# Optimization experiments

Hardware: AMD Instinct MI355X
Metric: run time of the kernel (lower is better)

The kernel has to match this reference:

```python
import jax, jax.numpy as jnp
import numpy as np
from jax import lax
from jax.scipy.special import logsumexp

B, S, H = 64, 512, 768
NUM_TAG, NUM_POS = 17, 45


def setup_inputs() -> dict:
    key = jax.random.key(0)
    ks = jax.random.split(key, 12)
    return {
        "hidden": jax.random.normal(ks[0], (B, S, H), dtype=jnp.float32),
        "mask": jnp.ones((B, S), dtype=jnp.int32),
        "target_tag": jax.random.randint(ks[1], (B, S), 0, NUM_TAG).astype(jnp.int64),
        "target_pos": jax.random.randint(ks[2], (B, S), 0, NUM_POS).astype(jnp.int64),
        "W_tag": jax.random.normal(ks[3], (H, NUM_TAG), dtype=jnp.float32) * 0.02,
        "b_tag": jnp.zeros((NUM_TAG,), dtype=jnp.float32),
        "W_pos": jax.random.normal(ks[4], (H, NUM_POS), dtype=jnp.float32) * 0.02,
        "b_pos": jnp.zeros((NUM_POS,), dtype=jnp.float32),
        "start_tag": jax.random.normal(ks[5], (NUM_TAG,), dtype=jnp.float32) * 0.1,
        "trans_tag": jax.random.normal(ks[6], (NUM_TAG, NUM_TAG), dtype=jnp.float32) * 0.1,
        "end_tag": jax.random.normal(ks[7], (NUM_TAG,), dtype=jnp.float32) * 0.1,
        "start_pos": jax.random.normal(ks[8], (NUM_POS,), dtype=jnp.float32) * 0.1,
        "trans_pos": jax.random.normal(ks[9], (NUM_POS, NUM_POS), dtype=jnp.float32) * 0.1,
        "end_pos": jax.random.normal(ks[10], (NUM_POS,), dtype=jnp.float32) * 0.1,
    }


def crf_nll(emissions, tags, mask, start, trans, end):
    """torchcrf negative log-likelihood, reduction='mean'. emissions:[B,S,T]."""
    e = jnp.swapaxes(emissions, 0, 1)            # [S,B,T]
    tg = jnp.swapaxes(tags, 0, 1)                # [S,B]
    m = jnp.swapaxes(mask, 0, 1).astype(emissions.dtype)  # [S,B]
    # --- numerator: score of the target path ---
    first = start[tg[0]] + jnp.take_along_axis(e[0], tg[0][:, None], 1)[:, 0]

    def num_step(carry, x):
        prev_tag, score = carry
        et, tt, mt = x
        s = trans[prev_tag, tt] + jnp.take_along_axis(et, tt[:, None], 1)[:, 0]
        score = score + s * mt
        prev_tag = jnp.where(mt > 0, tt, prev_tag)
        return (prev_tag, score), None

    (last_tag, num), _ = lax.scan(num_step, (tg[0], first), (e[1:], tg[1:], m[1:]))
    num = num + end[last_tag]
    # --- denominator: forward algorithm (log-sum-exp scan) ---
    score0 = start[None, :] + e[0]               # [B,T]

    def den_step(score, x):
        et, mt = x
        nxt = logsumexp(score[:, :, None] + trans[None, :, :] + et[:, None, :], axis=1)
        return jnp.where(mt[:, None] > 0, nxt, score), None

    den, _ = lax.scan(den_step, score0, (e[1:], m[1:]))
    den = logsumexp(den + end[None, :], axis=1)
    return -jnp.mean(num - den)


def crf_decode(emissions, mask, start, trans, end):
    """Viterbi decode; returns best tag paths [B,S] (int32)."""
    T = emissions.shape[-1]
    e = jnp.swapaxes(emissions, 0, 1)            # [S,B,T]
    m = jnp.swapaxes(mask, 0, 1)                 # [S,B]
    score0 = start[None, :] + e[0]

    def fwd_step(score, x):
        et, mt = x
        cand = score[:, :, None] + trans[None, :, :]     # [B,T,T]
        idx = jnp.argmax(cand, axis=1).astype(jnp.int32)  # [B,T] best prev tag
        nxt = jnp.max(cand, axis=1) + et
        keep = (mt > 0)[:, None]
        score = jnp.where(keep, nxt, score)
        idx = jnp.where(keep, idx, jnp.arange(T, dtype=jnp.int32)[None, :])
        return score, idx

    score, hist = lax.scan(fwd_step, score0, (e[1:], m[1:]))  # hist:[S-1,B,T]
    score = score + end[None, :]
    last = jnp.argmax(score, axis=1).astype(jnp.int32)        # [B]

    def back_step(tag, idx):
        prev = jnp.take_along_axis(idx, tag[:, None], 1)[:, 0]
        return prev, tag

    tag0, path = lax.scan(back_step, last, hist, reverse=True)  # path:[S-1,B]
    full = jnp.concatenate([tag0[None, :], path], axis=0)       # [S,B]
    return jnp.swapaxes(full, 0, 1)


def reference(hidden, mask, target_tag, target_pos,
              W_tag, b_tag, W_pos, b_pos,
              start_tag, trans_tag, end_tag,
              start_pos, trans_pos, end_pos):
    # dropout is identity in eval mode
    tag = jnp.einsum('bsh,ht->bst', hidden, W_tag) + b_tag   # [B,S,T]
    pos = jnp.einsum('bsh,hp->bsp', hidden, W_pos) + b_pos   # [B,S,P]
    loss_tag = crf_nll(jax.nn.log_softmax(tag, axis=2), target_tag, mask,
                       start_tag, trans_tag, end_tag)
    loss_pos = crf_nll(jax.nn.log_softmax(pos, axis=2), target_pos, mask,
                       start_pos, trans_pos, end_pos)
    pred_tag = crf_decode(tag, mask, start_tag, trans_tag, end_tag)
    pred_pos = crf_decode(pos, mask, start_pos, trans_pos, end_pos)
    return pred_tag, pred_pos, loss_tag, loss_pos
```

## Files before the change

### kernel.cpp

```cpp
#include <hip/hip_runtime.h>
#include <cmath>
#include <cstdint>
#include <cstddef>

#define NT 17
#define NP 45
#define CH 8

__device__ __forceinline__ float rlane(float v, int k) {
    return __int_as_float(__builtin_amdgcn_readlane(__float_as_int(v), k));
}

__device__ __forceinline__ float bperm(float v, int k) {
    return __int_as_float(__builtin_amdgcn_ds_bpermute(k * 4, __float_as_int(v)));
}

__device__ __forceinline__ void gload16(const float* g, float* l) {
    __builtin_amdgcn_global_load_lds(
        (const __attribute__((address_space(1))) void*)g,
        (__attribute__((address_space(3))) void*)l, 16, 0, 0);
}

__global__ __launch_bounds__(256) void pack_w(
    const float* __restrict__ Wt, const float* __restrict__ Wp,
    float* __restrict__ Wpk)
{
    int i = blockIdx.x * 256 + threadIdx.x;
    if (i >= 768 * 64) return;
    int k = i >> 6, c = i & 63;
    float v = 0.f;
    if (c < NT) v = Wt[k * NT + c];
    else if (c < NT + NP) v = Wp[k * NP + (c - NT)];
    Wpk[i] = v;
}

__global__ __launch_bounds__(256) void gemm_logits(
    const float* __restrict__ hidden, const float* __restrict__ Wpk,
    const float* __restrict__ bt, const float* __restrict__ bp,
    float* __restrict__ tagL, float* __restrict__ posL)
{
    __shared__ __align__(16) float As[64 * 32];
    __shared__ __align__(16) float Bs[32 * 64];
    const int tid = threadIdx.x;
    const int rg = tid >> 4;
    const int cg = tid & 15;
    const int srg = rg & 7;
    const int row0 = blockIdx.x * 64;

    float acc[4][4];
#pragma unroll
    for (int a = 0; a < 4; ++a)
#pragma unroll
        for (int b = 0; b < 4; ++b) acc[a][b] = 0.f;

    const int arow = tid >> 3;
    const int aq   = tid & 7;
    const int bk   = tid >> 4;
    const int bc4  = tid & 15;

#pragma unroll 1
    for (int kc = 0; kc < 768; kc += 32) {
        {
            int r0 = arow;
            int s0 = (r0 >> 2) & 7;
            gload16(hidden + (size_t)(row0 + r0) * 768 + kc + ((aq ^ s0) << 2),
                    As + r0 * 32 + aq * 4);
            int r1 = 32 + arow;
            int s1 = (r1 >> 2) & 7;
            gload16(hidden + (size_t)(row0 + r1) * 768 + kc + ((aq ^ s1) << 2),
                    As + r1 * 32 + aq * 4);
            gload16(Wpk + (size_t)(kc + bk) * 64 + bc4 * 4,
                    Bs + bk * 64 + bc4 * 4);
            gload16(Wpk + (size_t)(kc + 16 + bk) * 64 + bc4 * 4,
                    Bs + (16 + bk) * 64 + bc4 * 4);
        }
        __syncthreads();
#pragma unroll
        for (int k4 = 0; k4 < 8; ++k4) {
            const int qb = ((k4 ^ srg) << 2);
            float a_[4][4], b_[4][4];
#pragma unroll
            for (int jr = 0; jr < 4; ++jr) {
                float4 t = *(const float4*)(As + (rg * 4 + jr) * 32 + qb);
                a_[jr][0] = t.x; a_[jr][1] = t.y; a_[jr][2] = t.z; a_[jr][3] = t.w;
            }
#pragma unroll
            for (int kk = 0; kk < 4; ++kk) {
                float4 t = *(const float4*)(Bs + (k4 * 4 + kk) * 64 + cg * 4);
                b_[kk][0] = t.x; b_[kk][1] = t.y; b_[kk][2] = t.z; b_[kk][3] = t.w;
            }
#pragma unroll
            for (int kk = 0; kk < 4; ++kk)
#pragma unroll
                for (int jr = 0; jr < 4; ++jr)
#pragma unroll
                    for (int jc = 0; jc < 4; ++jc)
                        acc[jr][jc] = fmaf(a_[jr][kk], b_[kk][jc], acc[jr][jc]);
        }
        __syncthreads();
    }
#pragma unroll
    for (int jr = 0; jr < 4; ++jr) {
        size_t r = (size_t)row0 + rg * 4 + jr;
#pragma unroll
        for (int jc = 0; jc < 4; ++jc) {
            int c = cg * 4 + jc;
            if (c < NT) tagL[r * NT + c] = acc[jr][jc] + bt[c];
            else if (c < NT + NP) posL[r * NP + (c - NT)] = acc[jr][jc] + bp[c - NT];
        }
    }
}

template <int T, int PAD>
__device__ void nll_scan(int b,
    const float* __restrict__ logits, const int* __restrict__ mask,
    const int* __restrict__ targ, const float* __restrict__ start,
    const float* __restrict__ trans, const float* __restrict__ endv,
    float* __restrict__ den, float* __restrict__ num)
{
    const int lane = threadIdx.x;
    const int jj = (lane < T) ? lane : (T - 1);
    float Ecol[PAD];
#pragma unroll
    for (int i = 0; i < PAD; ++i) Ecol[i] = (i < T) ? __expf(trans[i * T + jj]) : 0.f;
    const float esjj = __expf(start[jj]);
    const float* eptr = logits + (size_t)b * 512 * T + jj;
    const int* mptr = mask + b * 512;

    float eb[CH], en[CH], fb[CH];
    int mb, mn = 0;
#pragma unroll
    for (int k = 0; k < CH; ++k) { eb[k] = eptr[k * T]; en[k] = 0.f; }
    mb = mptr[lane & (CH - 1)];

    float a = 0.f;
    int excorr = 0;
    for (int c = 0; c < 64; ++c) {
        unsigned long long kb = __ballot(mb > 0);
        if (c < 63) {
            const float* ep2 = eptr + (c + 1) * CH * T;
#pragma unroll
            for (int k = 0; k < CH; ++k) en[k] = ep2[k * T];
            mn = mptr[(c + 1) * CH + (lane & (CH - 1))];
        }
#pragma unroll
        for (int k = 0; k < CH; ++k) fb[k] = __expf(eb[k]);
#pragma unroll
        for (int s = 0; s < CH; ++s) {
            float bv[PAD];
#pragma unroll
            for (int i = 0; i < PAD; ++i) bv[i] = bperm(a, i);
            float d0 = 0.f, d1 = 0.f, d2 = 0.f, d3 = 0.f;
#pragma unroll
            for (int q = 0; q < PAD / 4; ++q) {
                d0 = fmaf(bv[4 * q + 0], Ecol[4 * q + 0], d0);
                d1 = fmaf(bv[4 * q + 1], Ecol[4 * q + 1], d1);
                d2 = fmaf(bv[4 * q + 2], Ecol[4 * q + 2], d2);
                d3 = fmaf(bv[4 * q + 3], Ecol[4 * q + 3], d3);
            }
            float cand = ((d0 + d1) + (d2 + d3)) * fb[s];
            bool keep = (kb >> s) & 1ULL;
            bool first = (c == 0) && (s == 0);
            a = first ? (esjj * fb[0]) : (keep ? cand : a);
        }
        float mv0 = rlane(a, 0), mv1 = rlane(a, 1);
        float mv2 = rlane(a, 2), mv3 = rlane(a, 3);
#pragma unroll
        for (int i = 4; i < T; i += 4) {
            mv0 = fmaxf(mv0, rlane(a, i + 0));
            mv1 = fmaxf(mv1, rlane(a, i + 1));
            mv2 = fmaxf(mv2, rlane(a, i + 2));
            mv3 = fmaxf(mv3, rlane(a, i + 3));
        }
        float m = fmaxf(fmaxf(mv0, mv1), fmaxf(mv2, mv3));
        int ex;
        (void)frexpf(m, &ex);
        a *= ldexpf(1.0f, -ex);
        excorr += ex;
#pragma unroll
        for (int k = 0; k < CH; ++k) eb[k] = en[k];
        mb = mn;
    }
    float term = (lane < T) ? a * __expf(endv[lane]) : 0.f;
#pragma unroll
    for (int o = 32; o; o >>= 1) term += __shfl_xor(term, o);
    if (lane == 0) den[b] = __logf(term) + (float)excorr * 0.69314718056f;

    float part = 0.f; int Lc = 0;
    for (int t = lane; t < 512; t += 64) {
        int mt = mask[b * 512 + t];
        Lc += (mt > 0);
        if (t >= 1 && mt > 0) {
            int tg = targ[b * 512 + t];
            int pg = targ[b * 512 + t - 1];
            part += trans[pg * T + tg] + logits[((size_t)b * 512 + t) * T + tg];
        }
    }
#pragma unroll
    for (int o = 32; o; o >>= 1) { part += __shfl_xor(part, o); Lc += __shfl_xor(Lc, o); }
    if (lane == 0) {
        int t0g = targ[b * 512];
        num[b] = start[t0g] + logits[(size_t)b * 512 * T + t0g]
               + part + endv[targ[b * 512 + Lc - 1]];
    }
}

template <int T, int PAD>
__device__ void vit_fwd(int b,
    const float* __restrict__ logits, const int* __restrict__ mask,
    const float* __restrict__ start, const float* __restrict__ trans,
    float* __restrict__ score)
{
    const int lane = threadIdx.x;
    const int jj = (lane < T) ? lane : (T - 1);
    float Tcol[PAD];
#pragma unroll
    for (int i = 0; i < PAD; ++i) Tcol[i] = (i < T) ? trans[i * T + jj] : -1e30f;
    const float sjj = start[jj];
    const float* eptr = logits + (size_t)b * 512 * T + jj;
    const int* mptr = mask + b * 512;
    float* sptr = score + (size_t)b * 512 * T + lane;

    float eb[CH], en[CH];
    int mb, mn = 0;
#pragma unroll
    for (int k = 0; k < CH; ++k) { eb[k] = eptr[k * T]; en[k] = 0.f; }
    mb = mptr[lane & (CH - 1)];

    float sc = 0.f;
    for (int c = 0; c < 64; ++c) {
        unsigned long long kb = __ballot(mb > 0);
        if (c < 63) {
            const float* ep2 = eptr + (c + 1) * CH * T;
#pragma unroll
            for (int k = 0; k < CH; ++k) en[k] = ep2[k * T];
            mn = mptr[(c + 1) * CH + (lane & (CH - 1))];
        }
#pragma unroll
        for (int s = 0; s < CH; ++s) {
            float bv[PAD];
#pragma unroll
            for (int i = 0; i < PAD; ++i) bv[i] = bperm(sc, i);
            float m = -1e30f;
#pragma unroll
            for (int q = 0; q < PAD / 4; ++q) {
                float ca = bv[4 * q + 0] + Tcol[4 * q + 0];
                float cb = bv[4 * q + 1] + Tcol[4 * q + 1];
                float cc = bv[4 * q + 2] + Tcol[4 * q + 2];
                float cd = bv[4 * q + 3] + Tcol[4 * q + 3];
                m = fmaxf(m, fmaxf(ca, cb));
                m = fmaxf(m, fmaxf(cc, cd));
            }
            float nxt = m + eb[s];
            bool keep = (kb >> s) & 1ULL;
            bool first = (c == 0) && (s == 0);
            sc = first ? (sjj + eb[0]) : (keep ? nxt : sc);
            if (lane < T) sptr[(size_t)(c * CH + s) * T] = sc;
        }
#pragma unroll
        for (int k = 0; k < CH; ++k) eb[k] = en[k];
        mb = mn;
    }
}

__global__ __launch_bounds__(64, 1) void scan_kernel(
    const float* tagL, const float* posL, const int* mask,
    const int* tgT, const int* tgP,
    const float* startT, const float* transT, const float* endT,
    const float* startP, const float* transP, const float* endP,
    float* scoreT, float* scoreP,
    float* denT, float* denP, float* numT, float* numP)
{
    int bid = blockIdx.x;
    if (bid < 64)
        vit_fwd<NP, 48>(bid, posL, mask, startP, transP, scoreP);
    else if (bid < 128)
        nll_scan<NP, 48>(bid - 64, posL, mask, tgP, startP, transP, endP, denP, numP);
    else if (bid < 192)
        vit_fwd<NT, 20>(bid - 128, tagL, mask, startT, transT, scoreT);
    else
        nll_scan<NT, 20>(bid - 192, tagL, mask, tgT, startT, transT, endT, denT, numT);
}

template <int T>
__device__ void hist_block(int b, int tc,
    const float* __restrict__ score, const int* __restrict__ mask,
    const float* __restrict__ trans, unsigned char* __restrict__ hist)
{
    const int wave = threadIdx.x >> 6;
    const int lane = threadIdx.x & 63;
    const int jj = (lane < T) ? lane : (T - 1);
    float Tcol[T];
#pragma unroll
    for (int i = 0; i < T; ++i) Tcol[i] = trans[i * T + jj];
    for (int q = 0; q < 16; ++q) {
        int t = tc * 64 + wave * 16 + q;
        if (t < 1) continue;
        int mt = mask[b * 512 + t];
        int hv;
        if (mt > 0) {
            float sv = score[((size_t)b * 512 + t - 1) * T + jj];
            float mx = -1e30f; int am = 0;
#pragma unroll
            for (int i = 0; i < T; ++i) {
                float cand = rlane(sv, i) + Tcol[i];
                bool g = cand > mx;
                mx = g ? cand : mx;
                am = g ? i : am;
            }
            hv = am;
        } else {
            hv = jj;
        }
        if (lane < T)
            hist[((size_t)b * 512 + (t - 1)) * T + lane] = (unsigned char)hv;
    }
}

__global__ __launch_bounds__(256) void hist_kernel(
    const float* scoreT, const float* scoreP, const int* mask,
    const float* transT, const float* transP,
    unsigned char* histT, unsigned char* histP)
{
    int blk = blockIdx.x;
    if (blk < 512) hist_block<NP>(blk >> 3, blk & 7, scoreP, mask, transP, histP);
    else { blk -= 512; hist_block<NT>(blk >> 3, blk & 7, scoreT, mask, transT, histT); }
}

template <int T>
__device__ void backtrace(int b, const float* __restrict__ score,
    const unsigned char* __restrict__ hist, const float* __restrict__ endv,
    float* __restrict__ outp, unsigned char* sh)
{
    unsigned char* h  = sh;
    unsigned char* g2 = sh + 512 * T;
    unsigned char* g4 = sh + 1024 * T;
    unsigned char* g8 = sh + 1024 * T + 128 * T;
    unsigned char* pr = sh + 1024 * T + 192 * T;
    const int lane = threadIdx.x;

    {
        const int4* src = (const int4*)(hist + (size_t)b * 512 * T);
        int4* dst = (int4*)h;
        int n16 = (512 * T) / 16;
        for (int i = lane; i < n16; i += 64) dst[i] = src[i];
    }
    __syncthreads();
    for (int idx = lane; idx < 510 * T; idx += 64) {
        int r = idx / T, i = idx - r * T;
        g2[idx] = h[r * T + h[(r + 1) * T + i]];
    }
    __syncthreads();
    for (int idx = lane; idx < 127 * T; idx += 64) {
        int a4 = idx / T, i = idx - a4 * T;
        int r = 3 + 4 * a4;
        g4[idx] = g2[r * T + g2[(r + 2) * T + i]];
    }
    __syncthreads();
    for (int idx = lane; idx < 63 * T; idx += 64) {
        int a = idx / T, i = idx - a * T;
        int r = 503 - 8 * a;
        int a4lo = (r - 3) >> 2, a4hi = (r + 1) >> 2;
        g8[idx] = g4[a4lo * T + g4[a4hi * T + i]];
    }
    float v = (lane < T) ? (score[((size_t)b * 512 + 511) * T + lane] + endv[lane]) : -1e30f;
    float mx = v;
#pragma unroll
    for (int o = 32; o; o >>= 1) mx = fmaxf(mx, __shfl_xor(mx, o));
    unsigned long long bal = __ballot(v == mx);
    int cur = __ffsll(bal) - 1;
    __syncthreads();
    int myCur = 0;
    for (int a = 0; a < 64; ++a) {
        if (lane == a) myCur = cur;
        if (a < 63) cur = g8[a * T + cur];
    }
    {
        int ta = 511 - 8 * lane;
        int j = myCur;
        pr[ta] = (unsigned char)j;
        int rlo = (lane == 63) ? 0 : (ta - 7);
        for (int r = ta - 1; r >= rlo; --r) {
            j = h[r * T + j];
            pr[r] = (unsigned char)j;
        }
    }
    __syncthreads();
    for (int k = lane; k < 512; k += 64)
        outp[(size_t)b * 512 + k] = (float)pr[k];
}

__global__ __launch_bounds__(64, 1) void backtrace_kernel(
    const float* scoreT, const float* scoreP,
    const unsigned char* histT, const unsigned char* histP,
    const float* endT, const float* endP,
    const float* numT, const float* denT,
    const float* numP, const float* denP, float* out)
{
    __shared__ __align__(16) unsigned char sh[1216 * NP + 576];
    int blk = blockIdx.x;
    if (blk < 64) backtrace<NP>(blk, scoreP, histP, endP, out + 32768, sh);
    else if (blk < 128) backtrace<NT>(blk - 64, scoreT, histT, endT, out, sh);
    else {
        int lane = threadIdx.x;
        float dT = numT[lane] - denT[lane];
        float dP = numP[lane] - denP[lane];
#pragma unroll
        for (int o = 32; o; o >>= 1) { dT += __shfl_xor(dT, o); dP += __shfl_xor(dP, o); }
        if (lane == 0) {
            out[65536] = -dT / 64.f;
            out[65537] = -dP / 64.f;
        }
    }
}

extern "C" void kernel_launch(void* const* d_in, const int* in_sizes, int n_in,
                              void* d_out, int out_size, void* d_ws, size_t ws_size,
                              hipStream_t stream)
{
    const float* hidden = (const float*)d_in[0];
    const int*   mask   = (const int*)d_in[1];
    const int*   tgT    = (const int*)d_in[2];
    const int*   tgP    = (const int*)d_in[3];
    const float* Wt     = (const float*)d_in[4];
    const float* bt     = (const float*)d_in[5];
    const float* Wp     = (const float*)d_in[6];
    const float* bp     = (const float*)d_in[7];
    const float* startT = (const float*)d_in[8];
    const float* transT = (const float*)d_in[9];
    const float* endT   = (const float*)d_in[10];
    const float* startP = (const float*)d_in[11];
    const float* transP = (const float*)d_in[12];
    const float* endP   = (const float*)d_in[13];

    float* ws     = (float*)d_ws;
    float* tagL   = ws;
    float* posL   = tagL + 557056;
    float* scoreT = posL + 1474560;
    float* scoreP = scoreT + 557056;
    float* denT   = scoreP + 1474560;
    float* denP   = denT + 64;
    float* numT   = denP + 64;
    float* numP   = numT + 64;
    unsigned char* histT = (unsigned char*)(numP + 64);
    unsigned char* histP = histT + (size_t)64 * 512 * NT;
    float* out = (float*)d_out;

    float* Wpk = scoreT;

    pack_w<<<192, 256, 0, stream>>>(Wt, Wp, Wpk);
    gemm_logits<<<512, 256, 0, stream>>>(hidden, Wpk, bt, bp, tagL, posL);
    scan_kernel<<<256, 64, 0, stream>>>(tagL, posL, mask, tgT, tgP,
        startT, transT, endT, startP, transP, endP,
        scoreT, scoreP, denT, denP, numT, numP);
    hist_kernel<<<1024, 256, 0, stream>>>(scoreT, scoreP, mask, transT, transP,
        histT, histP);
    backtrace_kernel<<<129, 64, 0, stream>>>(scoreT, scoreP, histT, histP,
        endT, endP, numT, denT, numP, denP, out);
}
```

Baseline: 409.9 us.

## Fuse Viterbi backpointer argmax into forward scan and drop hist kernel

Result: slower. 494.1 us (+20.6%).

```diff
diff --git a/kernel.cpp b/kernel.cpp
--- a/kernel.cpp
+++ b/kernel.cpp
@@ -6,6 +6,7 @@
 #define NT 17
 #define NP 45
 #define CH 8
+#define HS 528
 
 __device__ __forceinline__ float rlane(float v, int k) {
     return __int_as_float(__builtin_amdgcn_readlane(__float_as_int(v), k));
@@ -209,8 +210,9 @@
 __device__ void vit_fwd(int b,
     const float* __restrict__ logits, const int* __restrict__ mask,
     const float* __restrict__ start, const float* __restrict__ trans,
-    float* __restrict__ score)
-{
+    float* __restrict__ scoreFin, unsigned char* __restrict__ histX)
+{
+    constexpr int L = PAD / 4;
     const int lane = threadIdx.x;
     const int jj = (lane < T) ? lane : (T - 1);
     float Tcol[PAD];
@@ -219,7 +221,7 @@
     const float sjj = start[jj];
     const float* eptr = logits + (size_t)b * 512 * T + jj;
     const int* mptr = mask + b * 512;
-    float* sptr = score + (size_t)b * 512 * T + lane;
+    unsigned char* hbase = histX + ((size_t)b * T + lane) * HS;
 
     float eb[CH], en[CH];
     int mb, mn = 0;
@@ -228,6 +230,7 @@
     mb = mptr[lane & (CH - 1)];
 
     float sc = 0.f;
+    unsigned int plo = 0, phi = 0;
     for (int c = 0; c < 64; ++c) {
         unsigned long long kb = __ballot(mb > 0);
         if (c < 63) {
@@ -241,25 +244,62 @@
             float bv[PAD];
 #pragma unroll
             for (int i = 0; i < PAD; ++i) bv[i] = bperm(sc, i);
+            float cnd[PAD];
+#pragma unroll
+            for (int i = 0; i < PAD; ++i) cnd[i] = bv[i] + Tcol[i];
             float m = -1e30f;
 #pragma unroll
             for (int q = 0; q < PAD / 4; ++q) {
-                float ca = bv[4 * q + 0] + Tcol[4 * q + 0];
-                float cb = bv[4 * q + 1] + Tcol[4 * q + 1];
-                float cc = bv[4 * q + 2] + Tcol[4 * q + 2];
-                float cd = bv[4 * q + 3] + Tcol[4 * q + 3];
-                m = fmaxf(m, fmaxf(ca, cb));
-                m = fmaxf(m, fmaxf(cc, cd));
-            }
-            float nxt = m + eb[s];
+                m = fmaxf(m, fmaxf(cnd[4 * q + 0], cnd[4 * q + 1]));
+                m = fmaxf(m, fmaxf(cnd[4 * q + 2], cnd[4 * q + 3]));
+            }
+            float mc0 = cnd[0];         int ac0 = 0;
+            float mc1 = cnd[L];         int ac1 = L;
+            float mc2 = cnd[2 * L];     int ac2 = 2 * L;
+            float mc3 = cnd[3 * L];     int ac3 = 3 * L;
+#pragma unroll
+            for (int i = 1; i < L; ++i) {
+                float c0 = cnd[i];          bool g0 = c0 > mc0;
+                mc0 = g0 ? c0 : mc0;        ac0 = g0 ? i : ac0;
+                float c1 = cnd[L + i];      bool g1 = c1 > mc1;
+                mc1 = g1 ? c1 : mc1;        ac1 = g1 ? (L + i) : ac1;
+                float c2 = cnd[2 * L + i];  bool g2 = c2 > mc2;
+                mc2 = g2 ? c2 : mc2;        ac2 = g2 ? (2 * L + i) : ac2;
+                float c3 = cnd[3 * L + i];  bool g3 = c3 > mc3;
+                mc3 = g3 ? c3 : mc3;        ac3 = g3 ? (3 * L + i) : ac3;
+            }
+            float mx = mc0; int am = ac0;
+            { bool g = mc1 > mx; mx = g ? mc1 : mx; am = g ? ac1 : am; }
+            { bool g = mc2 > mx; mx = g ? mc2 : mx; am = g ? ac2 : am; }
+            { bool g = mc3 > mx; mx = g ? mc3 : mx; am = g ? ac3 : am; }
+
             bool keep = (kb >> s) & 1ULL;
             bool first = (c == 0) && (s == 0);
+            float nxt = m + eb[s];
             sc = first ? (sjj + eb[0]) : (keep ? nxt : sc);
-            if (lane < T) sptr[(size_t)(c * CH + s) * T] = sc;
+            int hv = keep ? am : jj;
+            if (s == 0) {
+                if (c > 0) {
+                    phi |= (unsigned)hv << 24;
+                    if (lane < T)
+                        *(unsigned long long*)(hbase + (c * CH - 8)) =
+                            ((unsigned long long)phi << 32) | plo;
+                    plo = 0; phi = 0;
+                }
+            } else if (s <= 4) {
+                plo |= (unsigned)hv << (8 * (s - 1));
+            } else {
+                phi |= (unsigned)hv << (8 * (s - 5));
+            }
         }
 #pragma unroll
         for (int k = 0; k < CH; ++k) eb[k] = en[k];
         mb = mn;
+    }
+    if (lane < T) {
+        *(unsigned long long*)(hbase + 504) =
+            ((unsigned long long)phi << 32) | plo;
+        scoreFin[b * 64 + lane] = sc;
     }
 }
 
@@ -268,87 +308,43 @@
     const int* tgT, const int* tgP,
     const float* startT, const float* transT, const float* endT,
     const float* startP, const float* transP, const float* endP,
-    float* scoreT, float* scoreP,
+    float* scFT, float* scFP,
+    unsigned char* histXT, unsigned char* histXP,
     float* denT, float* denP, float* numT, float* numP)
 {
     int bid = blockIdx.x;
     if (bid < 64)
-        vit_fwd<NP, 48>(bid, posL, mask, startP, transP, scoreP);
+        vit_fwd<NP, 48>(bid, posL, mask, startP, transP, scFP, histXP);
     else if (bid < 128)
         nll_scan<NP, 48>(bid - 64, posL, mask, tgP, startP, transP, endP, denP, numP);
     else if (bid < 192)
-        vit_fwd<NT, 20>(bid - 128, tagL, mask, startT, transT, scoreT);
+        vit_fwd<NT, 20>(bid - 128, tagL, mask, startT, transT, scFT, histXT);
     else
         nll_scan<NT, 20>(bid - 192, tagL, mask, tgT, startT, transT, endT, denT, numT);
 }
 
 template <int T>
-__device__ void hist_block(int b, int tc,
-    const float* __restrict__ score, const int* __restrict__ mask,
-    const float* __restrict__ trans, unsigned char* __restrict__ hist)
-{
-    const int wave = threadIdx.x >> 6;
-    const int lane = threadIdx.x & 63;
-    const int jj = (lane < T) ? lane : (T - 1);
-    float Tcol[T];
-#pragma unroll
-    for (int i = 0; i < T; ++i) Tcol[i] = trans[i * T + jj];
-    for (int q = 0; q < 16; ++q) {
-        int t = tc * 64 + wave * 16 + q;
-        if (t < 1) continue;
-        int mt = mask[b * 512 + t];
-        int hv;
-        if (mt > 0) {
-            float sv = score[((size_t)b * 512 + t - 1) * T + jj];
-            float mx = -1e30f; int am = 0;
-#pragma unroll
-            for (int i = 0; i < T; ++i) {
-                float cand = rlane(sv, i) + Tcol[i];
-                bool g = cand > mx;
-                mx = g ? cand : mx;
-                am = g ? i : am;
-            }
-            hv = am;
-        } else {
-            hv = jj;
-        }
-        if (lane < T)
-            hist[((size_t)b * 512 + (t - 1)) * T + lane] = (unsigned char)hv;
-    }
-}
-
-__global__ __launch_bounds__(256) void hist_kernel(
-    const float* scoreT, const float* scoreP, const int* mask,
-    const float* transT, const float* transP,
-    unsigned char* histT, unsigned char* histP)
-{
-    int blk = blockIdx.x;
-    if (blk < 512) hist_block<NP>(blk >> 3, blk & 7, scoreP, mask, transP, histP);
-    else { blk -= 512; hist_block<NT>(blk >> 3, blk & 7, scoreT, mask, transT, histT); }
-}
-
-template <int T>
-__device__ void backtrace(int b, const float* __restrict__ score,
-    const unsigned char* __restrict__ hist, const float* __restrict__ endv,
+__device__ void backtrace(int b, const float* __restrict__ scoreFin,
+    const unsigned char* __restrict__ histX, const float* __restrict__ endv,
     float* __restrict__ outp, unsigned char* sh)
 {
     unsigned char* h  = sh;
-    unsigned char* g2 = sh + 512 * T;
-    unsigned char* g4 = sh + 1024 * T;
-    unsigned char* g8 = sh + 1024 * T + 128 * T;
-    unsigned char* pr = sh + 1024 * T + 192 * T;
+    unsigned char* g2 = sh + HS * T;
+    unsigned char* g4 = sh + (HS + 512) * T;
+    unsigned char* g8 = sh + (HS + 640) * T;
+    unsigned char* pr = sh + (HS + 704) * T;
     const int lane = threadIdx.x;
 
     {
-        const int4* src = (const int4*)(hist + (size_t)b * 512 * T);
+        const int4* src = (const int4*)(histX + (size_t)b * T * HS);
         int4* dst = (int4*)h;
-        int n16 = (512 * T) / 16;
+        int n16 = (T * HS) / 16;
         for (int i = lane; i < n16; i += 64) dst[i] = src[i];
     }
     __syncthreads();
     for (int idx = lane; idx < 510 * T; idx += 64) {
         int r = idx / T, i = idx - r * T;
-        g2[idx] = h[r * T + h[(r + 1) * T + i]];
+        g2[idx] = h[(int)h[i * HS + (r + 1)] * HS + r];
     }
     __syncthreads();
     for (int idx = lane; idx < 127 * T; idx += 64) {
@@ -363,7 +359,7 @@
         int a4lo = (r - 3) >> 2, a4hi = (r + 1) >> 2;
         g8[idx] = g4[a4lo * T + g4[a4hi * T + i]];
     }
-    float v = (lane < T) ? (score[((size_t)b * 512 + 511) * T + lane] + endv[lane]) : -1e30f;
+    float v = (lane < T) ? (scoreFin[b * 64 + lane] + endv[lane]) : -1e30f;
     float mx = v;
 #pragma unroll
     for (int o = 32; o; o >>= 1) mx = fmaxf(mx, __shfl_xor(mx, o));
@@ -381,7 +377,7 @@
         pr[ta] = (unsigned char)j;
         int rlo = (lane == 63) ? 0 : (ta - 7);
         for (int r = ta - 1; r >= rlo; --r) {
-            j = h[r * T + j];
+            j = h[j * HS + r];
             pr[r] = (unsigned char)j;
         }
     }
@@ -391,16 +387,16 @@
 }
 
 __global__ __launch_bounds__(64, 1) void backtrace_kernel(
-    const float* scoreT, const float* scoreP,
-    const unsigned char* histT, const unsigned char* histP,
+    const float* scFT, const float* scFP,
+    const unsigned char* histXT, const unsigned char* histXP,
     const float* endT, const float* endP,
     const float* numT, const float* denT,
     const float* numP, const float* denP, float* out)
 {
-    __shared__ __align__(16) unsigned char sh[1216 * NP + 576];
+    __shared__ __align__(16) unsigned char sh[(HS + 704) * NP + 512];
     int blk = blockIdx.x;
-    if (blk < 64) backtrace<NP>(blk, scoreP, histP, endP, out + 32768, sh);
-    else if (blk < 128) backtrace<NT>(blk - 64, scoreT, histT, endT, out, sh);
+    if (blk < 64) backtrace<NP>(blk, scFP, histXP, endP, out + 32768, sh);
+    else if (blk < 128) backtrace<NT>(blk - 64, scFT, histXT, endT, out, sh);
     else {
         int lane = threadIdx.x;
         float dT = numT[lane] - denT[lane];
@@ -433,28 +429,25 @@
     const float* transP = (const float*)d_in[12];
     const float* endP   = (const float*)d_in[13];
 
-    float* ws     = (float*)d_ws;
-    float* tagL   = ws;
-    float* posL   = tagL + 557056;
-    float* scoreT = posL + 1474560;
-    float* scoreP = scoreT + 557056;
-    float* denT   = scoreP + 1474560;
-    float* denP   = denT + 64;
-    float* numT   = denP + 64;
-    float* numP   = numT + 64;
-    unsigned char* histT = (unsigned char*)(numP + 64);
-    unsigned char* histP = histT + (size_t)64 * 512 * NT;
+    float* ws   = (float*)d_ws;
+    float* tagL = ws;
+    float* posL = tagL + 557056;
+    float* Wpk  = posL + 1474560;
+    float* denT = Wpk + 49152;
+    float* denP = denT + 64;
+    float* numT = denP + 64;
+    float* numP = numT + 64;
+    float* scFT = numP + 64;
+    float* scFP = scFT + 4096;
+    unsigned char* histXT = (unsigned char*)(scFP + 4096);
+    unsigned char* histXP = histXT + (size_t)64 * NT * HS;
     float* out = (float*)d_out;
-
-    float* Wpk = scoreT;
 
     pack_w<<<192, 256, 0, stream>>>(Wt, Wp, Wpk);
     gemm_logits<<<512, 256, 0, stream>>>(hidden, Wpk, bt, bp, tagL, posL);
     scan_kernel<<<256, 64, 0, stream>>>(tagL, posL, mask, tgT, tgP,
         startT, transT, endT, startP, transP, endP,
-        scoreT, scoreP, denT, denP, numT, numP);
-    hist_kernel<<<1024, 256, 0, stream>>>(scoreT, scoreP, mask, transT, transP,
-        histT, histP);
-    backtrace_kernel<<<129, 64, 0, stream>>>(scoreT, scoreP, histT, histP,
+        scFT, scFP, histXT, histXP, denT, denP, numT, numP);
+    backtrace_kernel<<<129, 64, 0, stream>>>(scFT, scFP, histXT, histXP,
         endT, endP, numT, denT, numP, denP, out);
 }
```
